# Performance work log

Measured on AMD Instinct MI355X. Metric: run time of the kernel, lower is better.

The kernel has to match this reference:

```python
import jax, jax.numpy as jnp
import numpy as np

B, L, H, NH, D, I = 2, 2048, 2048, 16, 128, 8192
EPS = 1e-6
ROPE_BASE = 10000.0


def rms_norm(x, w):
    x32 = x.astype(jnp.float32)
    n = x32 * jax.lax.rsqrt(jnp.mean(x32 * x32, axis=-1, keepdims=True) + EPS)
    return (n * w).astype(x.dtype)


def rope(x, offset):
    # x: [B, L, H, D], non-traditional (half-split) RoPE
    d = x.shape[-1]
    half = d // 2
    inv_freq = 1.0 / (ROPE_BASE ** (jnp.arange(half, dtype=jnp.float32) * 2.0 / d))
    pos = jnp.arange(x.shape[1], dtype=jnp.float32) + offset
    ang = pos[:, None] * inv_freq[None, :]              # [L, half]
    cos = jnp.cos(ang)[None, :, None, :]
    sin = jnp.sin(ang)[None, :, None, :]
    x1, x2 = x[..., :half], x[..., half:]
    out = jnp.concatenate([x1 * cos - x2 * sin, x2 * cos + x1 * sin], axis=-1)
    return out.astype(x.dtype)


def setup_inputs() -> dict:
    key = jax.random.key(0)
    ks = jax.random.split(key, 9)
    s = 0.02
    causal = jnp.where(jnp.tril(jnp.ones((L, L), dtype=bool)), 0.0, -1e9).astype(jnp.float32)
    return {
        "x": jax.random.normal(ks[0], (B, L, H), dtype=jnp.float32),
        "ln1_w": jnp.ones((H,), dtype=jnp.float32),
        "ln2_w": jnp.ones((H,), dtype=jnp.float32),
        "wq": jax.random.normal(ks[1], (H, H), dtype=jnp.float32) * s,
        "wk": jax.random.normal(ks[2], (H, H), dtype=jnp.float32) * s,
        "wv": jax.random.normal(ks[3], (H, H), dtype=jnp.float32) * s,
        "wo": jax.random.normal(ks[4], (H, H), dtype=jnp.float32) * s,
        "w_gate": jax.random.normal(ks[5], (I, H), dtype=jnp.float32) * s,
        "w_up": jax.random.normal(ks[6], (I, H), dtype=jnp.float32) * s,
        "w_down": jax.random.normal(ks[7], (H, I), dtype=jnp.float32) * s,
        "mask": causal,
        "offset": 0,
    }


def reference(x, ln1_w, ln2_w, wq, wk, wv, wo, w_gate, w_up, w_down, mask, offset):
    residual = x
    h = rms_norm(x, ln1_w)
    # QKV projections (torch Linear: y = x @ W.T)
    q = jnp.einsum("ble,oe->blo", h, wq).reshape(B, L, NH, D)
    k = jnp.einsum("ble,oe->blo", h, wk).reshape(B, L, NH, D)
    v = jnp.einsum("ble,oe->blo", h, wv).reshape(B, L, NH, D)
    q = rope(q, offset)
    k = rope(k, offset)
    # [B, NH, L, D]
    q = q.transpose(0, 2, 1, 3)
    k = k.transpose(0, 2, 1, 3)
    v = v.transpose(0, 2, 1, 3)
    scores = jnp.einsum("bhqd,bhkd->bhqk", q.astype(jnp.float32), k.astype(jnp.float32))
    scores = scores / np.sqrt(D).astype(np.float32)
    if mask is not None:
        scores = scores + mask
    probs = jax.nn.softmax(scores, axis=-1).astype(v.dtype)
    attn = jnp.einsum("bhqk,bhkd->bhqd", probs, v)
    attn = attn.transpose(0, 2, 1, 3).reshape(B, L, NH * D)
    h = jnp.einsum("blo,eo->ble", attn, wo)
    x = h + residual
    residual = x
    h = rms_norm(x, ln2_w)
    gate = jax.nn.silu(jnp.einsum("ble,ie->bli", h, w_gate))
    up = jnp.einsum("ble,ie->bli", h, w_up)
    mlp = jnp.einsum("bli,ei->ble", gate * up, w_down)
    return mlp + residual
```

## Files before the change

kernel.cpp:

```cpp
#include <hip/hip_runtime.h>
#include <stdint.h>

#define B_ 2
#define L_ 2048
#define H_ 2048
#define NH_ 16
#define D_ 128
#define I_ 8192
#define M_ (B_*L_)

typedef unsigned short u16;
typedef __attribute__((ext_vector_type(8))) short bf16x8;
typedef __attribute__((ext_vector_type(4))) float f32x4;

__device__ __forceinline__ u16 f2bf(float f) {
  union { float f; uint32_t u; } c; c.f = f;
  return (u16)((c.u + 0x7fffu + ((c.u >> 16) & 1u)) >> 16);
}
__device__ __forceinline__ float bf2f(u16 h) {
  union { uint32_t u; float f; } c; c.u = ((uint32_t)h) << 16;
  return c.f;
}
__device__ __forceinline__ void gload16(const void* g, void* l) {
  __builtin_amdgcn_global_load_lds(
      (__attribute__((address_space(1))) void*)g,
      (__attribute__((address_space(3))) void*)l, 16, 0, 0);
}

__global__ void cvt_w(const float* __restrict__ src, u16* __restrict__ dst, int n4) {
  int i = blockIdx.x * blockDim.x + threadIdx.x;
  if (i >= n4) return;
  float4 v = ((const float4*)src)[i];
  ushort4 o;
  o.x = f2bf(v.x); o.y = f2bf(v.y); o.z = f2bf(v.z); o.w = f2bf(v.w);
  ((ushort4*)dst)[i] = o;
}

__global__ __launch_bounds__(256) void down_reduce(const u16* __restrict__ p0,
                                                   const u16* __restrict__ p1,
                                                   const float* __restrict__ res,
                                                   float* __restrict__ out, int n4) {
  int i = blockIdx.x * blockDim.x + threadIdx.x;
  if (i >= n4) return;
  ushort4 a = ((const ushort4*)p0)[i];
  ushort4 b = ((const ushort4*)p1)[i];
  float4 r = ((const float4*)res)[i];
  float4 o;
  o.x = bf2f(a.x) + bf2f(b.x) + r.x;
  o.y = bf2f(a.y) + bf2f(b.y) + r.y;
  o.z = bf2f(a.z) + bf2f(b.z) + r.z;
  o.w = bf2f(a.w) + bf2f(b.w) + r.w;
  ((float4*)out)[i] = o;
}

__global__ __launch_bounds__(256)
void reduce_rms(const u16* __restrict__ p0, const u16* __restrict__ p1,
                const float* __restrict__ res, const float* __restrict__ w,
                float* __restrict__ x2o, u16* __restrict__ h2o) {
  int row = blockIdx.x, t = threadIdx.x;
  size_t base = (size_t)row * H_;
  ushort4 a0 = ((const ushort4*)(p0 + base))[t * 2];
  ushort4 a1 = ((const ushort4*)(p0 + base))[t * 2 + 1];
  ushort4 b0 = ((const ushort4*)(p1 + base))[t * 2];
  ushort4 b1 = ((const ushort4*)(p1 + base))[t * 2 + 1];
  float4 r0 = ((const float4*)(res + base))[t * 2];
  float4 r1 = ((const float4*)(res + base))[t * 2 + 1];
  float4 v0, v1;
  v0.x = bf2f(a0.x) + bf2f(b0.x) + r0.x;
  v0.y = bf2f(a0.y) + bf2f(b0.y) + r0.y;
  v0.z = bf2f(a0.z) + bf2f(b0.z) + r0.z;
  v0.w = bf2f(a0.w) + bf2f(b0.w) + r0.w;
  v1.x = bf2f(a1.x) + bf2f(b1.x) + r1.x;
  v1.y = bf2f(a1.y) + bf2f(b1.y) + r1.y;
  v1.z = bf2f(a1.z) + bf2f(b1.z) + r1.z;
  v1.w = bf2f(a1.w) + bf2f(b1.w) + r1.w;
  ((float4*)(x2o + base))[t * 2] = v0;
  ((float4*)(x2o + base))[t * 2 + 1] = v1;
  float s = v0.x*v0.x + v0.y*v0.y + v0.z*v0.z + v0.w*v0.w
          + v1.x*v1.x + v1.y*v1.y + v1.z*v1.z + v1.w*v1.w;
  for (int m = 1; m < 64; m <<= 1) s += __shfl_xor(s, m);
  __shared__ float sm[4];
  if ((t & 63) == 0) sm[t >> 6] = s;
  __syncthreads();
  float tot = sm[0] + sm[1] + sm[2] + sm[3];
  float rs = rsqrtf(tot / (float)H_ + 1e-6f);
  const float4* wr = (const float4*)w;
  float4 w0 = wr[t * 2], w1 = wr[t * 2 + 1];
  ushort4 o0, o1;
  o0.x = f2bf(v0.x * rs * w0.x); o0.y = f2bf(v0.y * rs * w0.y);
  o0.z = f2bf(v0.z * rs * w0.z); o0.w = f2bf(v0.w * rs * w0.w);
  o1.x = f2bf(v1.x * rs * w1.x); o1.y = f2bf(v1.y * rs * w1.y);
  o1.z = f2bf(v1.z * rs * w1.z); o1.w = f2bf(v1.w * rs * w1.w);
  ((ushort4*)(h2o + base))[t * 2] = o0;
  ((ushort4*)(h2o + base))[t * 2 + 1] = o1;
}

__global__ __launch_bounds__(256) void rmsnorm_k(const float* __restrict__ x,
                                                 const float* __restrict__ w,
                                                 u16* __restrict__ out) {
  int row = blockIdx.x;
  int t = threadIdx.x;
  const float4* xr = (const float4*)(x + (size_t)row * H_);
  float4 a = xr[t * 2], b = xr[t * 2 + 1];
  float s = a.x*a.x + a.y*a.y + a.z*a.z + a.w*a.w
          + b.x*b.x + b.y*b.y + b.z*b.z + b.w*b.w;
  for (int m = 1; m < 64; m <<= 1) s += __shfl_xor(s, m);
  __shared__ float sm[4];
  if ((t & 63) == 0) sm[t >> 6] = s;
  __syncthreads();
  float tot = sm[0] + sm[1] + sm[2] + sm[3];
  float rs = rsqrtf(tot / (float)H_ + 1e-6f);
  const float4* wr = (const float4*)w;
  float4 w0 = wr[t * 2], w1 = wr[t * 2 + 1];
  ushort4 o0, o1;
  o0.x = f2bf(a.x * rs * w0.x); o0.y = f2bf(a.y * rs * w0.y);
  o0.z = f2bf(a.z * rs * w0.z); o0.w = f2bf(a.w * rs * w0.w);
  o1.x = f2bf(b.x * rs * w1.x); o1.y = f2bf(b.y * rs * w1.y);
  o1.z = f2bf(b.z * rs * w1.z); o1.w = f2bf(b.w * rs * w1.w);
  ushort4* orow = (ushort4*)(out + (size_t)row * H_);
  orow[t * 2] = o0; orow[t * 2 + 1] = o1;
}

__global__ void rope_tab(float* __restrict__ cosT, float* __restrict__ sinT,
                         const int* __restrict__ offp) {
  int i = blockIdx.x * blockDim.x + threadIdx.x;
  int d = i & 63, l = i >> 6;
  float inv = powf(10000.0f, -(float)d / 64.0f);
  float ang = (float)(l + *offp) * inv;
  cosT[i] = cosf(ang);
  sinT[i] = sinf(ang);
}

__global__ void rope_apply(u16* __restrict__ qk, const float* __restrict__ cosT,
                           const float* __restrict__ sinT) {
  int i = blockIdx.x * blockDim.x + threadIdx.x;
  int d = i & 63;
  size_t row = (size_t)(i >> 6);
  int l = (int)(row & (L_ - 1));
  u16* p = qk + row * D_;
  float x1 = bf2f(p[d]), x2 = bf2f(p[d + 64]);
  float c = cosT[l * 64 + d], s = sinT[l * 64 + d];
  p[d]      = f2bf(x1 * c - x2 * s);
  p[d + 64] = f2bf(x2 * c + x1 * s);
}

__global__ __launch_bounds__(256) void vtrans_k(const u16* __restrict__ v,
                                                u16* __restrict__ vt) {
  __shared__ u16 tile[64][65];
  int l0 = blockIdx.x * 64, d0 = blockIdx.y * 64;
  size_t base = (size_t)blockIdx.z * L_ * D_;
  int t = threadIdx.x;
  int tr = t >> 3, tc = (t & 7) * 8;
  #pragma unroll
  for (int it = 0; it < 2; ++it) {
    int r = tr + it * 32;
    const u16* src = v + base + (size_t)(l0 + r) * D_ + d0 + tc;
    ushort4 u0 = ((const ushort4*)src)[0], u1 = ((const ushort4*)src)[1];
    tile[r][tc + 0] = u0.x; tile[r][tc + 1] = u0.y;
    tile[r][tc + 2] = u0.z; tile[r][tc + 3] = u0.w;
    tile[r][tc + 4] = u1.x; tile[r][tc + 5] = u1.y;
    tile[r][tc + 6] = u1.z; tile[r][tc + 7] = u1.w;
  }
  __syncthreads();
  #pragma unroll
  for (int it = 0; it < 2; ++it) {
    int r = tr + it * 32;
    u16* dst = vt + base + (size_t)(d0 + r) * L_ + l0 + tc;
    ushort4 o0, o1;
    o0.x = tile[tc + 0][r]; o0.y = tile[tc + 1][r];
    o0.z = tile[tc + 2][r]; o0.w = tile[tc + 3][r];
    o1.x = tile[tc + 4][r]; o1.y = tile[tc + 5][r];
    o1.z = tile[tc + 6][r]; o1.w = tile[tc + 7][r];
    ((ushort4*)dst)[0] = o0; ((ushort4*)dst)[1] = o1;
  }
}

#define EPI_SILU 1
#define EPI_MUL 2
#define EPI_PART 4
#define EPI_QKV3 5
#define EPI_GLU 6

template <int EPI>
__global__ __launch_bounds__(512, 2)
void gemm256(const u16* __restrict__ A, const u16* __restrict__ Bw,
             int M, int N, int K, int nk,
             u16* __restrict__ outb, u16* __restrict__ outb2,
             const u16* __restrict__ Bw2) {
  __shared__ __attribute__((aligned(16))) u16 Asm[2][2][8192];
  __shared__ __attribute__((aligned(16))) u16 Bsm[2][2][8192];
  int tid = threadIdx.x;
  int wid = tid >> 6, lane = tid & 63;
  int r16 = lane & 15, g4 = lane >> 4;
  int nwg = gridDim.x, bid = blockIdx.x;
  int q8 = nwg >> 3, r8 = nwg & 7, xcd = bid & 7, loc = bid >> 3;
  int wgall = (xcd < r8 ? xcd * (q8 + 1) : r8 * (q8 + 1) + (xcd - r8) * q8) + loc;
  int nwg_geo = (M >> 8) * ((EPI == EPI_GLU) ? (N >> 7) : (N >> 8));
  int ks = wgall / nwg_geo;
  int wg = wgall % nwg_geo;
  int MX = M >> 8;
  int m0 = (wg % MX) * 256;
  int n0 = (wg / MX) * ((EPI == EPI_GLU) ? 128 : 256);
  const char* Ab = (const char*)(A + (size_t)ks * nk * 64);
  const char* Bb = (const char*)(Bw + (size_t)ks * nk * 64);
  const char* Bb2 = (const char*)Bw2;
  u16* ob = (EPI == EPI_PART && ks) ? outb2 : outb;

  f32x4 acc[2][2][4][2] = {};
  bf16x8 afr[4][2];
  bf16x8 bfr[2][2][2];

  auto STAGE = [&](int kt1, int sel) {
    if (kt1 >= nk) return;
    int buf = kt1 & 1;
    int k0 = kt1 << 6;
    const char* gb; char* lb; int row0;
    if (sel == 0)      { gb = Ab; row0 = m0;       lb = (char*)&Asm[buf][0][0]; }
    else if (sel == 3) { gb = Ab; row0 = m0 + 128; lb = (char*)&Asm[buf][1][0]; }
    else if (sel == 1) { gb = Bb; row0 = n0;       lb = (char*)&Bsm[buf][0][0]; }
    else               { gb = (EPI == EPI_GLU) ? Bb2 : Bb;
                         row0 = (EPI == EPI_GLU) ? n0 : n0 + 128;
                         lb = (char*)&Bsm[buf][1][0]; }
    #pragma unroll
    for (int j = 0; j < 2; ++j) {
      int p = j * 8192 + wid * 1024 + lane * 16;
      int r = p >> 7;
      int cb = (p & 127) ^ ((r & 7) << 4);
      gload16(gb + ((size_t)(row0 + r) * K + k0) * 2 + cb,
              lb + j * 8192 + wid * 1024);
    }
  };

  STAGE(0, 0); STAGE(0, 1); STAGE(0, 2); STAGE(0, 3);

  const int QM[4] = {0, 0, 1, 1};
  const int QN[4] = {0, 1, 1, 0};

  for (int kt = 0; kt < nk; ++kt) {
    int cur = kt & 1;
    #pragma unroll
    for (int ph = 0; ph < 4; ++ph) {
      if (ph < 3) {
        __builtin_amdgcn_sched_barrier(0);
        asm volatile("s_waitcnt vmcnt(4)" ::: "memory");
      }
      __builtin_amdgcn_s_barrier();
      __builtin_amdgcn_sched_barrier(0);
      const int qm = QM[ph], qn = QN[ph];
      if (ph == 0 || ph == 2) {
        const char* Ah = (const char*)&Asm[cur][qm][0];
        #pragma unroll
        for (int mf = 0; mf < 4; ++mf) {
          int R = (wid >> 2) * 64 + mf * 16 + r16;
          int sw = (R & 7) << 4;
          afr[mf][0] = *(const bf16x8*)(Ah + R * 128 + ((g4 * 16) ^ sw));
          afr[mf][1] = *(const bf16x8*)(Ah + R * 128 + ((64 + g4 * 16) ^ sw));
        }
      }
      if (ph == 0 || ph == 1) {
        const char* Bh = (const char*)&Bsm[cur][qn][0];
        #pragma unroll
        for (int nf = 0; nf < 2; ++nf) {
          int R = (wid & 3) * 32 + nf * 16 + r16;
          int sw = (R & 7) << 4;
          bfr[qn][nf][0] = *(const bf16x8*)(Bh + R * 128 + ((g4 * 16) ^ sw));
          bfr[qn][nf][1] = *(const bf16x8*)(Bh + R * 128 + ((64 + g4 * 16) ^ sw));
        }
      }
      STAGE(kt + 1, ph);
      __builtin_amdgcn_s_setprio(1);
      #pragma unroll
      for (int mf = 0; mf < 4; ++mf)
        #pragma unroll
        for (int nf = 0; nf < 2; ++nf)
          #pragma unroll
          for (int kk = 0; kk < 2; ++kk)
            acc[qm][qn][mf][nf] = __builtin_amdgcn_mfma_f32_16x16x32_bf16(
                afr[mf][kk], bfr[qn][nf][kk], acc[qm][qn][mf][nf], 0, 0, 0);
      __builtin_amdgcn_s_setprio(0);
    }
  }
  if (EPI == EPI_GLU) {
    #pragma unroll
    for (int qm = 0; qm < 2; ++qm)
      #pragma unroll
      for (int mf = 0; mf < 4; ++mf)
        #pragma unroll
        for (int nf = 0; nf < 2; ++nf)
          #pragma unroll
          for (int rr = 0; rr < 4; ++rr) {
            int row = m0 + qm * 128 + (wid >> 2) * 64 + mf * 16 + g4 * 4 + rr;
            int col = n0 + (wid & 3) * 32 + nf * 16 + r16;
            float g = acc[qm][0][mf][nf][rr];
            float u = acc[qm][1][mf][nf][rr];
            float sg = g / (1.0f + __expf(-g));
            outb[(size_t)row * N + col] = f2bf(sg * u);
          }
    return;
  }
  #pragma unroll
  for (int qm = 0; qm < 2; ++qm)
    #pragma unroll
    for (int qn = 0; qn < 2; ++qn)
      #pragma unroll
      for (int mf = 0; mf < 4; ++mf)
        #pragma unroll
        for (int nf = 0; nf < 2; ++nf)
          #pragma unroll
          for (int rr = 0; rr < 4; ++rr) {
            int row = m0 + qm * 128 + (wid >> 2) * 64 + mf * 16 + g4 * 4 + rr;
            int col = n0 + qn * 128 + (wid & 3) * 32 + nf * 16 + r16;
            float val = acc[qm][qn][mf][nf][rr];
            if (EPI == EPI_SILU) {
              ob[(size_t)row * N + col] = f2bf(val / (1.0f + __expf(-val)));
            } else if (EPI == EPI_MUL) {
              float g = bf2f(ob[(size_t)row * N + col]);
              ob[(size_t)row * N + col] = f2bf(g * val);
            } else if (EPI == EPI_PART) {
              ob[(size_t)row * N + col] = f2bf(val);
            } else if (EPI == EPI_QKV3) {
              int which = col >> 11, within = col & 2047;
              int hh = within >> 7, d = within & 127;
              int bb = row >> 11, l = row & 2047;
              ob[(size_t)which * M_ * H_ +
                 ((((size_t)bb * NH_ + hh) * L_ + l) << 7) + d] = f2bf(val);
            }
          }
}

__global__ __launch_bounds__(256)
void flash_attn(const u16* __restrict__ q, const u16* __restrict__ k,
                const u16* __restrict__ vt, u16* __restrict__ out) {
  __shared__ __attribute__((aligned(16))) u16 Kt[2][64 * 128];
  __shared__ __attribute__((aligned(16))) u16 Vt[2][128 * 64];
  __shared__ __attribute__((aligned(16))) u16 Pl[4][16 * 64];
  int tid = threadIdx.x, w = tid >> 6, lane = tid & 63;
  int r16 = lane & 15, g4 = lane >> 4;
  int b = blockIdx.z, h = blockIdx.y;
  int qt = gridDim.x - 1 - blockIdx.x;
  int q0 = qt * 64;
  size_t bh = (size_t)b * NH_ + h;
  const char* qb = (const char*)(q + bh * L_ * D_);
  const char* kb = (const char*)(k + bh * L_ * D_);
  const char* vb = (const char*)(vt + bh * D_ * L_);
  int qrow = q0 + w * 16 + r16;
  bf16x8 qf[4];
  #pragma unroll
  for (int c = 0; c < 4; ++c)
    qf[c] = *(const bf16x8*)(qb + ((size_t)qrow * 128 + c * 32 + g4 * 8) * 2);
  f32x4 oacc[8] = {};
  float mrow[4], lsum[4];
  #pragma unroll
  for (int r = 0; r < 4; ++r) { mrow[r] = -3.0e38f; lsum[r] = 0.f; }
  int myq = q0 + w * 16 + g4 * 4;
  int ntiles = qt + 1;
  int rsw = (r16 & 7) << 4;
  const float sc = 0.08838834764831845f;

  auto STAGEKV = [&](int t, int buf) {
    if (t >= ntiles) return;
    int kv0 = t * 64;
    #pragma unroll
    for (int i = 0; i < 4; ++i) {
      int uoff = i * 4096 + w * 1024;
      int lin = uoff + lane * 16;
      int krow = lin >> 8;
      int kcol = (lin & 255) ^ ((krow & 7) << 4);
      gload16(kb + (size_t)(kv0 + krow) * 256 + kcol,
              (char*)&Kt[buf][0] + uoff);
      int vrow = lin >> 7;
      int vcol = (lin & 127) ^ ((vrow & 7) << 4);
      gload16(vb + (size_t)vrow * (L_ * 2) + kv0 * 2 + vcol,
              (char*)&Vt[buf][0] + uoff);
    }
  };

  STAGEKV(0, 0);
  __syncthreads();

  for (int t = 0; t < ntiles; ++t) {
    int buf = t & 1;
    int kv0 = t * 64;
    STAGEKV(t + 1, buf ^ 1);
    const char* Kb = (const char*)&Kt[buf][0];
    const char* Vb = (const char*)&Vt[buf][0];
    f32x4 s[4] = {};
    __builtin_amdgcn_s_setprio(1);
    #pragma unroll
    for (int c = 0; c < 4; ++c) {
      #pragma unroll
      for (int n = 0; n < 4; ++n) {
        bf16x8 kf = *(const bf16x8*)(Kb + (n * 16 + r16) * 256
                                     + ((c * 64 + g4 * 16) ^ rsw));
        s[n] = __builtin_amdgcn_mfma_f32_16x16x32_bf16(qf[c], kf, s[n], 0, 0, 0);
      }
    }
    __builtin_amdgcn_s_setprio(0);
    #pragma unroll
    for (int r = 0; r < 4; ++r) {
      float rm = -3.0e38f;
      #pragma unroll
      for (int n = 0; n < 4; ++n) {
        float v = s[n][r] * sc;
        int kvi = kv0 + n * 16 + r16;
        if (kvi > myq + r) v = -3.0e38f;
        s[n][r] = v;
        rm = fmaxf(rm, v);
      }
      rm = fmaxf(rm, __shfl_xor(rm, 1));
      rm = fmaxf(rm, __shfl_xor(rm, 2));
      rm = fmaxf(rm, __shfl_xor(rm, 4));
      rm = fmaxf(rm, __shfl_xor(rm, 8));
      float mnew = fmaxf(mrow[r], rm);
      float alpha = __expf(mrow[r] - mnew);
      mrow[r] = mnew;
      lsum[r] *= alpha;
      #pragma unroll
      for (int nf = 0; nf < 8; ++nf) oacc[nf][r] *= alpha;
      int prow = g4 * 4 + r;
      int psw = (prow & 7) << 3;
      #pragma unroll
      for (int n = 0; n < 4; ++n) {
        float pv = __expf(s[n][r] - mnew);
        lsum[r] += pv;
        Pl[w][prow * 64 + ((n * 16 + r16) ^ psw)] = f2bf(pv);
      }
    }
    asm volatile("s_waitcnt lgkmcnt(0)" ::: "memory");
    __builtin_amdgcn_sched_barrier(0);
    __builtin_amdgcn_s_setprio(1);
    #pragma unroll
    for (int kc = 0; kc < 2; ++kc) {
      bf16x8 pf = *(const bf16x8*)((const char*)&Pl[w][0] + r16 * 128
                                   + ((kc * 64 + g4 * 16) ^ rsw));
      #pragma unroll
      for (int nf = 0; nf < 8; ++nf) {
        bf16x8 vf = *(const bf16x8*)(Vb + (nf * 16 + r16) * 128
                                     + ((kc * 64 + g4 * 16) ^ rsw));
        oacc[nf] = __builtin_amdgcn_mfma_f32_16x16x32_bf16(pf, vf, oacc[nf], 0, 0, 0);
      }
    }
    __builtin_amdgcn_s_setprio(0);
    __syncthreads();
  }
  #pragma unroll
  for (int r = 0; r < 4; ++r) {
    float l = lsum[r];
    l += __shfl_xor(l, 1); l += __shfl_xor(l, 2);
    l += __shfl_xor(l, 4); l += __shfl_xor(l, 8);
    float inv = 1.0f / l;
    size_t orow = ((size_t)b * L_ + (myq + r)) * H_ + h * D_;
    #pragma unroll
    for (int nf = 0; nf < 8; ++nf)
      out[orow + nf * 16 + r16] = f2bf(oacc[nf][r] * inv);
  }
}

extern "C" void kernel_launch(void* const* d_in, const int* in_sizes, int n_in,
                              void* d_out, int out_size, void* d_ws, size_t ws_size,
                              hipStream_t stream) {
  (void)in_sizes; (void)n_in; (void)out_size;
  const float* x    = (const float*)d_in[0];
  const float* ln1w = (const float*)d_in[1];
  const float* ln2w = (const float*)d_in[2];
  const float* wq   = (const float*)d_in[3];
  const float* wk   = (const float*)d_in[4];
  const float* wv   = (const float*)d_in[5];
  const float* wo   = (const float*)d_in[6];
  const float* wg   = (const float*)d_in[7];
  const float* wu   = (const float*)d_in[8];
  const float* wd   = (const float*)d_in[9];
  const int*   offp = (const int*)d_in[11];
  float* out = (float*)d_out;

  char* p = (char*)d_ws;
  auto alloc = [&](size_t bytes) {
    char* r = p;
    p += (bytes + 255) & ~(size_t)255;
    return r;
  };
  const size_t HH = (size_t)H_ * H_, IH = (size_t)I_ * H_;
  u16* wbuf = (u16*)alloc(IH * 2);
  u16* h1   = (u16*)alloc((size_t)M_ * H_ * 2);
  u16* qb   = (u16*)alloc((size_t)M_ * H_ * 2);
  u16* kb   = (u16*)alloc((size_t)M_ * H_ * 2);
  u16* vb   = (u16*)alloc((size_t)M_ * H_ * 2);
  u16* vtb  = (u16*)alloc((size_t)M_ * H_ * 2);
  u16* attn = (u16*)alloc((size_t)M_ * H_ * 2);
  float* x2 = (float*)alloc((size_t)M_ * H_ * 4);
  float* cosT = (float*)alloc((size_t)L_ * 64 * 4);
  float* sinT = (float*)alloc((size_t)L_ * 64 * 4);
  u16* h2    = h1;
  u16* gateb = qb;
  u16* wu_b = (u16*)alloc(IH * 2);
  bool fused_glu = ((char*)wu_b + IH * 2) <= ((char*)d_ws + ws_size);

  const int nHH4 = (int)(HH / 4), nIH4 = (int)(IH / 4);
  const int MH4 = M_ * H_ / 4;

  rmsnorm_k<<<M_, 256, 0, stream>>>(x, ln1w, h1);
  rope_tab<<<(L_ * 64) / 256, 256, 0, stream>>>(cosT, sinT, offp);

  cvt_w<<<nHH4 / 256, 256, 0, stream>>>(wq, wbuf, nHH4);
  cvt_w<<<nHH4 / 256, 256, 0, stream>>>(wk, wbuf + HH, nHH4);
  cvt_w<<<nHH4 / 256, 256, 0, stream>>>(wv, wbuf + 2 * HH, nHH4);
  int nwg_qkv = (M_ / 256) * (3 * H_ / 256);
  gemm256<EPI_QKV3><<<nwg_qkv, 512, 0, stream>>>(h1, wbuf, M_, 3 * H_, H_,
                                                 H_ / 64, qb, nullptr, nullptr);

  int nrope = B_ * NH_ * L_ * 64;
  rope_apply<<<nrope / 256, 256, 0, stream>>>(qb, cosT, sinT);
  rope_apply<<<nrope / 256, 256, 0, stream>>>(qb + (size_t)M_ * H_, cosT, sinT);
  vtrans_k<<<dim3(L_ / 64, D_ / 64, B_ * NH_), 256, 0, stream>>>(
      qb + 2 * (size_t)M_ * H_, vtb);

  flash_attn<<<dim3(L_ / 64, NH_, B_), 256, 0, stream>>>(
      qb, qb + (size_t)M_ * H_, vtb, attn);

  cvt_w<<<nHH4 / 256, 256, 0, stream>>>(wo, wbuf, nHH4);
  int nwg_wo = 2 * (M_ / 256) * (H_ / 256);
  gemm256<EPI_PART><<<nwg_wo, 512, 0, stream>>>(attn, wbuf, M_, H_, H_,
                                                H_ / 128, kb, vb, nullptr);
  reduce_rms<<<M_, 256, 0, stream>>>(kb, vb, x, ln2w, x2, h2);

  if (fused_glu) {
    cvt_w<<<nIH4 / 256, 256, 0, stream>>>(wg, wbuf, nIH4);
    cvt_w<<<nIH4 / 256, 256, 0, stream>>>(wu, wu_b, nIH4);
    int nwg_glu = (M_ / 256) * (I_ / 128);
    gemm256<EPI_GLU><<<nwg_glu, 512, 0, stream>>>(h2, wbuf, M_, I_, H_,
                                                  H_ / 64, gateb, nullptr, wu_b);
  } else {
    int nwg256 = (M_ / 256) * (I_ / 256);
    cvt_w<<<nIH4 / 256, 256, 0, stream>>>(wg, wbuf, nIH4);
    gemm256<EPI_SILU><<<nwg256, 512, 0, stream>>>(h2, wbuf, M_, I_, H_,
                                                  H_ / 64, gateb, nullptr, nullptr);
    cvt_w<<<nIH4 / 256, 256, 0, stream>>>(wu, wbuf, nIH4);
    gemm256<EPI_MUL><<<nwg256, 512, 0, stream>>>(h2, wbuf, M_, I_, H_,
                                                 H_ / 64, gateb, nullptr, nullptr);
  }

  cvt_w<<<nIH4 / 256, 256, 0, stream>>>(wd, wbuf, nIH4);
  int nwg_dn = 2 * (M_ / 256) * (H_ / 256);
  gemm256<EPI_PART><<<nwg_dn, 512, 0, stream>>>(gateb, wbuf, M_, H_, I_,
                                                I_ / 128, h1, attn, nullptr);
  down_reduce<<<MH4 / 256, 256, 0, stream>>>(h1, attn, x2, out, MH4);
}
```

Measured before the change: 792.5 us.

## Split-K QKV GEMM with fused reduce+RoPE finish kernel and merged weight conversion

When workspace allows, the QKV projection now runs as a split-K GEMM (768 workgroups, two bf16 partial buffers). A new qkv_finish kernel sums the partials, applies RoPE to Q and K, and writes Q/K/V, replacing the separate rope_apply launches. The three Q/K/V weight conversions are merged into one cvt3 launch, and the later split-K grid sizes become literal constants. The aim is more parallelism for the QKV GEMM and fewer launches, at the cost of extra partial-buffer traffic and a non-vectorized finish kernel.

```diff
diff --git a/kernel.cpp b/kernel.cpp
--- a/kernel.cpp
+++ b/kernel.cpp
@@ -34,6 +34,47 @@
   ushort4 o;
   o.x = f2bf(v.x); o.y = f2bf(v.y); o.z = f2bf(v.z); o.w = f2bf(v.w);
   ((ushort4*)dst)[i] = o;
+}
+
+__global__ void cvt3(const float* __restrict__ s0, const float* __restrict__ s1,
+                     const float* __restrict__ s2, u16* __restrict__ dst, int n4) {
+  int i = blockIdx.x * blockDim.x + threadIdx.x;
+  int reg = i / n4, off = i % n4;
+  const float* src = (reg == 0) ? s0 : (reg == 1) ? s1 : s2;
+  float4 v = ((const float4*)src)[off];
+  ushort4 o;
+  o.x = f2bf(v.x); o.y = f2bf(v.y); o.z = f2bf(v.z); o.w = f2bf(v.w);
+  ((ushort4*)(dst + (size_t)reg * H_ * H_))[off] = o;
+}
+
+__global__ __launch_bounds__(256)
+void qkv_finish(const u16* __restrict__ p0, const u16* __restrict__ p1,
+                const float* __restrict__ cosT, const float* __restrict__ sinT,
+                u16* __restrict__ qb, u16* __restrict__ kb, u16* __restrict__ vb) {
+  int i = blockIdx.x * blockDim.x + threadIdx.x;
+  int d = i & 63;
+  size_t row = (size_t)(i >> 6);
+  int l = (int)(row & (L_ - 1));
+  int h = (int)((row >> 11) & (NH_ - 1));
+  int b = (int)(row >> 15);
+  size_t bl = (size_t)b * L_ + l;
+  const u16* r0 = p0 + bl * (3 * H_);
+  const u16* r1 = p1 + bl * (3 * H_);
+  int c = h * 128 + d;
+  float cv = cosT[l * 64 + d], sv = sinT[l * 64 + d];
+  float x1 = bf2f(r0[c]) + bf2f(r1[c]);
+  float x2 = bf2f(r0[c + 64]) + bf2f(r1[c + 64]);
+  u16* qp = qb + row * D_;
+  qp[d]      = f2bf(x1 * cv - x2 * sv);
+  qp[d + 64] = f2bf(x2 * cv + x1 * sv);
+  x1 = bf2f(r0[c + 2048]) + bf2f(r1[c + 2048]);
+  x2 = bf2f(r0[c + 2112]) + bf2f(r1[c + 2112]);
+  u16* kp = kb + row * D_;
+  kp[d]      = f2bf(x1 * cv - x2 * sv);
+  kp[d + 64] = f2bf(x2 * cv + x1 * sv);
+  u16* vp = vb + row * D_;
+  vp[d]      = f2bf(bf2f(r0[c + 4096]) + bf2f(r1[c + 4096]));
+  vp[d + 64] = f2bf(bf2f(r0[c + 4160]) + bf2f(r1[c + 4160]));
 }
 
 __global__ __launch_bounds__(256) void down_reduce(const u16* __restrict__ p0,
@@ -492,8 +533,18 @@
   float* sinT = (float*)alloc((size_t)L_ * 64 * 4);
   u16* h2    = h1;
   u16* gateb = qb;
-  u16* wu_b = (u16*)alloc(IH * 2);
-  bool fused_glu = ((char*)wu_b + IH * 2) <= ((char*)d_ws + ws_size);
+  size_t used_base = (size_t)(p - (char*)d_ws);
+  size_t MB96 = 2 * (((size_t)M_ * 3 * H_ * 2 + 255) & ~(size_t)255);
+  bool tier1 = (used_base + MB96) <= ws_size;
+  bool tier2 = !tier1 && (used_base + IH * 2) <= ws_size;
+  u16 *p0 = nullptr, *p1 = nullptr, *wu_b = nullptr;
+  if (tier1) {
+    p0 = (u16*)alloc((size_t)M_ * 3 * H_ * 2);
+    p1 = (u16*)alloc((size_t)M_ * 3 * H_ * 2);
+    wu_b = p0;
+  } else if (tier2) {
+    wu_b = (u16*)alloc(IH * 2);
+  }
 
   const int nHH4 = (int)(HH / 4), nIH4 = (int)(IH / 4);
   const int MH4 = M_ * H_ / 4;
@@ -501,29 +552,31 @@
   rmsnorm_k<<<M_, 256, 0, stream>>>(x, ln1w, h1);
   rope_tab<<<(L_ * 64) / 256, 256, 0, stream>>>(cosT, sinT, offp);
 
-  cvt_w<<<nHH4 / 256, 256, 0, stream>>>(wq, wbuf, nHH4);
-  cvt_w<<<nHH4 / 256, 256, 0, stream>>>(wk, wbuf + HH, nHH4);
-  cvt_w<<<nHH4 / 256, 256, 0, stream>>>(wv, wbuf + 2 * HH, nHH4);
-  int nwg_qkv = (M_ / 256) * (3 * H_ / 256);
-  gemm256<EPI_QKV3><<<nwg_qkv, 512, 0, stream>>>(h1, wbuf, M_, 3 * H_, H_,
-                                                 H_ / 64, qb, nullptr, nullptr);
-
-  int nrope = B_ * NH_ * L_ * 64;
-  rope_apply<<<nrope / 256, 256, 0, stream>>>(qb, cosT, sinT);
-  rope_apply<<<nrope / 256, 256, 0, stream>>>(qb + (size_t)M_ * H_, cosT, sinT);
-  vtrans_k<<<dim3(L_ / 64, D_ / 64, B_ * NH_), 256, 0, stream>>>(
-      qb + 2 * (size_t)M_ * H_, vtb);
-
-  flash_attn<<<dim3(L_ / 64, NH_, B_), 256, 0, stream>>>(
-      qb, qb + (size_t)M_ * H_, vtb, attn);
+  cvt3<<<3 * nHH4 / 256, 256, 0, stream>>>(wq, wk, wv, wbuf, nHH4);
+
+  if (tier1) {
+    gemm256<EPI_PART><<<768, 512, 0, stream>>>(h1, wbuf, M_, 3 * H_, H_,
+                                               H_ / 128, p0, p1, nullptr);
+    qkv_finish<<<(B_ * NH_ * L_ * 64) / 256, 256, 0, stream>>>(
+        p0, p1, cosT, sinT, qb, kb, vb);
+  } else {
+    int nwg_qkv = (M_ / 256) * (3 * H_ / 256);
+    gemm256<EPI_QKV3><<<nwg_qkv, 512, 0, stream>>>(h1, wbuf, M_, 3 * H_, H_,
+                                                   H_ / 64, qb, nullptr, nullptr);
+    int nrope = B_ * NH_ * L_ * 64;
+    rope_apply<<<nrope / 256, 256, 0, stream>>>(qb, cosT, sinT);
+    rope_apply<<<nrope / 256, 256, 0, stream>>>(kb, cosT, sinT);
+  }
+
+  vtrans_k<<<dim3(L_ / 64, D_ / 64, B_ * NH_), 256, 0, stream>>>(vb, vtb);
+  flash_attn<<<dim3(L_ / 64, NH_, B_), 256, 0, stream>>>(qb, kb, vtb, attn);
 
   cvt_w<<<nHH4 / 256, 256, 0, stream>>>(wo, wbuf, nHH4);
-  int nwg_wo = 2 * (M_ / 256) * (H_ / 256);
-  gemm256<EPI_PART><<<nwg_wo, 512, 0, stream>>>(attn, wbuf, M_, H_, H_,
-                                                H_ / 128, kb, vb, nullptr);
+  gemm256<EPI_PART><<<256, 512, 0, stream>>>(attn, wbuf, M_, H_, H_,
+                                             H_ / 128, kb, vb, nullptr);
   reduce_rms<<<M_, 256, 0, stream>>>(kb, vb, x, ln2w, x2, h2);
 
-  if (fused_glu) {
+  if (tier1 || tier2) {
     cvt_w<<<nIH4 / 256, 256, 0, stream>>>(wg, wbuf, nIH4);
     cvt_w<<<nIH4 / 256, 256, 0, stream>>>(wu, wu_b, nIH4);
     int nwg_glu = (M_ / 256) * (I_ / 128);
@@ -540,8 +593,7 @@
   }
 
   cvt_w<<<nIH4 / 256, 256, 0, stream>>>(wd, wbuf, nIH4);
-  int nwg_dn = 2 * (M_ / 256) * (H_ / 256);
-  gemm256<EPI_PART><<<nwg_dn, 512, 0, stream>>>(gateb, wbuf, M_, H_, I_,
-                                                I_ / 128, h1, attn, nullptr);
+  gemm256<EPI_PART><<<256, 512, 0, stream>>>(gateb, wbuf, M_, H_, I_,
+                                             I_ / 128, h1, attn, nullptr);
   down_reduce<<<MH4 / 256, 256, 0, stream>>>(h1, attn, x2, out, MH4);
 }
```

Result: no change. 784.9 us (median of 2 runs) (-1.0%).
